# Performance work log

Hardware: AMD Instinct MI355X
Metric: run time of the kernel (lower is better)

Reference implementation:

```python
import jax, jax.numpy as jnp
import numpy as np

# ---- static config (mirrors GptOssDecoderLayer init) ----
H = 1024      # hidden_size
HD = 64       # head_size
NQ = 16       # num_query_heads
NKV = 4       # num_key_value_heads
G = NQ // NKV # num_key_value_groups
E = 8         # num_experts
TOPK = 2      # experts_per_token
FFN = 1024    # expert intermediate (== hidden in GPT-OSS)
B, Q = 4, 128 # batch sequences, new query tokens per sequence
P, PS = 8, 128
S = P * PS    # kv length per sequence
T = B * Q     # total query tokens
SW = 128      # sliding window (layer_idx % 2 == 0 -> active)
LIMIT = 7.0   # swiglu_limit
ALPHA = 1.702
EPS = 1e-5
NEG = -1e30
SCALE = HD ** -0.5


def rmsnorm(x, w):
    return x * w * jax.lax.rsqrt(jnp.mean(x * x, axis=-1, keepdims=True) + EPS)


def setup_inputs() -> dict:
    key = jax.random.key(0)
    ks = jax.random.split(key, 16)
    hidden = jax.random.normal(ks[0], (T, H), jnp.float32)
    kv_cache = jax.random.normal(ks[1], (B * P, 2, PS, NKV, HD), jnp.float32)
    kv_page_indices = jnp.arange(B * P, dtype=jnp.int32).reshape(B, P)
    # additive causal mask: query q sits at absolute position S - Q + q
    qpos = S - Q + jnp.arange(Q)
    kpos = jnp.arange(S)
    causal = qpos[:, None] >= kpos[None, :]
    attention_mask = jnp.broadcast_to(
        jnp.where(causal, 0.0, NEG).astype(jnp.float32), (B, Q, S))
    sinks = 0.1 * jax.random.normal(ks[2], (NQ,), jnp.float32)
    w_qkv = jax.random.normal(ks[3], (H, HD * (NQ + 2 * NKV)), jnp.float32) / np.sqrt(H)
    b_qkv = jnp.zeros((HD * (NQ + 2 * NKV),), jnp.float32)
    w_o = jax.random.normal(ks[4], (NQ * HD, H), jnp.float32) / np.sqrt(NQ * HD)
    b_o = jnp.zeros((H,), jnp.float32)
    ln1_w = jnp.ones((H,), jnp.float32)
    ln2_w = jnp.ones((H,), jnp.float32)
    w_router = jax.random.normal(ks[5], (H, E), jnp.float32) / np.sqrt(H)
    b_router = jnp.zeros((E,), jnp.float32)
    w_gate_up = jax.random.normal(ks[6], (E, H, 2 * FFN), jnp.float32) / np.sqrt(H)
    b_gate_up = jnp.zeros((E, 2 * FFN), jnp.float32)
    w_down = jax.random.normal(ks[7], (E, FFN, H), jnp.float32) / np.sqrt(FFN)
    b_down = jnp.zeros((E, H), jnp.float32)
    return dict(hidden=hidden, kv_cache=kv_cache, attention_mask=attention_mask,
                kv_page_indices=kv_page_indices, sinks=sinks, w_qkv=w_qkv,
                b_qkv=b_qkv, w_o=w_o, b_o=b_o, ln1_w=ln1_w, ln2_w=ln2_w,
                w_router=w_router, b_router=b_router, w_gate_up=w_gate_up,
                b_gate_up=b_gate_up, w_down=w_down, b_down=b_down)


def reference(hidden, kv_cache, attention_mask, kv_page_indices, sinks,
              w_qkv, b_qkv, w_o, b_o, ln1_w, ln2_w, w_router, b_router,
              w_gate_up, b_gate_up, w_down, b_down):
    # ---- attention block ----
    x = rmsnorm(hidden, ln1_w)
    qkv = x @ w_qkv + b_qkv                       # [T, HD*(NQ+2*NKV)]
    q = qkv[:, :NQ * HD].reshape(B, Q, NQ, HD)
    k_new = qkv[:, NQ * HD:(NQ + NKV) * HD].reshape(B, Q, NKV, HD)
    v_new = qkv[:, (NQ + NKV) * HD:].reshape(B, Q, NKV, HD)
    # gather paged KV cache -> [B, S, NKV, HD]; write new tokens into tail slots
    pages = kv_cache[kv_page_indices]             # [B, P, 2, PS, NKV, HD]
    K = pages[:, :, 0].reshape(B, S, NKV, HD).at[:, S - Q:].set(k_new)
    V = pages[:, :, 1].reshape(B, S, NKV, HD).at[:, S - Q:].set(v_new)
    Kr = jnp.repeat(K, G, axis=2)                 # GQA expand -> [B, S, NQ, HD]
    Vr = jnp.repeat(V, G, axis=2)
    scores = jnp.einsum('bqhd,bshd->bhqs', q * SCALE, Kr) + attention_mask[:, None]
    # sliding-window (module trims pages outside the window; equivalent mask)
    qpos = S - Q + jnp.arange(Q)
    kpos = jnp.arange(S)
    win_ok = (qpos[:, None] - kpos[None, :]) < SW
    scores = jnp.where(win_ok[None, None], scores, NEG)
    m = jnp.max(scores, axis=-1)
    m = jnp.where(jnp.isinf(m) & (m < 0), 0.0, m)
    p = jnp.exp(scores - m[..., None])            # [B, NQ, Q, S]
    # attention sink joins the softmax denominator (online-softmax correction)
    denom = jnp.sum(p, axis=-1) + jnp.exp(sinks[None, :, None] - m)
    attn = jnp.einsum('bhqs,bshd->bhqd', p, Vr) / denom[..., None]
    attn = attn.transpose(0, 2, 1, 3).reshape(T, NQ * HD)
    h = hidden + attn @ w_o + b_o
    # ---- MoE block ----
    x2 = rmsnorm(h, ln2_w)
    logits = x2 @ w_router + b_router             # [T, E]
    vals, idx = jax.lax.top_k(logits, TOPK)
    wts = jax.nn.softmax(vals, axis=-1)
    comb = jnp.sum(jax.nn.one_hot(idx, E, dtype=x2.dtype) * wts[..., None], axis=1)
    gu = jnp.einsum('th,ehf->etf', x2, w_gate_up) + b_gate_up[:, None, :]
    gate = jnp.minimum(gu[..., 0::2], LIMIT)
    up = jnp.clip(gu[..., 1::2], -LIMIT, LIMIT)
    glu = gate * jax.nn.sigmoid(gate * ALPHA)
    eo = jnp.einsum('etf,efh->eth', (up + 1.0) * glu, w_down) + b_down[:, None, :]
    moe = jnp.einsum('te,eth->th', comb, eo)
    return h + moe
```

## Files before the change

kernel.cpp:

```cpp
#include <hip/hip_runtime.h>

constexpr int H    = 1024;
constexpr int HD   = 64;
constexpr int NQ   = 16;
constexpr int NKV  = 4;
constexpr int E_   = 8;
constexpr int FFN  = 1024;
constexpr int B_   = 4;
constexpr int Q_   = 128;
constexpr int P_   = 8;
constexpr int PS   = 128;
constexpr int S_   = P_ * PS;
constexpr int T_   = B_ * Q_;
constexpr int QKV_N = HD * (NQ + 2 * NKV);
constexpr float EPS   = 1e-5f;
constexpr float ALPHA = 1.702f;
constexpr float LIMIT = 7.0f;
constexpr float SCALE = 0.125f;

constexpr int MAXROWS = 1536;
constexpr int MAXTILES = 24;

typedef __attribute__((ext_vector_type(4))) float f32x4;
typedef __attribute__((ext_vector_type(8))) short s16x8;

__device__ __forceinline__ unsigned short f2bf(float f) {
    unsigned u = __float_as_uint(f);
    u += 0x7FFFu + ((u >> 16) & 1u);
    return (unsigned short)(u >> 16);
}

__device__ __forceinline__ void lds_barrier() {
    asm volatile("s_waitcnt lgkmcnt(0)" ::: "memory");
    __builtin_amdgcn_s_barrier();
}

__global__ __launch_bounds__(256) void rmsnorm_kernel(const float* __restrict__ in,
                                                      const float* __restrict__ w,
                                                      unsigned short* __restrict__ outb,
                                                      int* __restrict__ cnt) {
    int t   = blockIdx.x;
    int tid = threadIdx.x;
    if (t == 0 && tid < E_) cnt[tid] = 0;
    float4 v = ((const float4*)(in + (size_t)t * H))[tid];
    float ss = v.x * v.x + v.y * v.y + v.z * v.z + v.w * v.w;
#pragma unroll
    for (int off = 32; off; off >>= 1) ss += __shfl_down(ss, off);
    __shared__ float partial[4];
    __shared__ float s_inv;
    if ((tid & 63) == 0) partial[tid >> 6] = ss;
    __syncthreads();
    if (tid == 0)
        s_inv = rsqrtf((partial[0] + partial[1] + partial[2] + partial[3]) * (1.0f / H) + EPS);
    __syncthreads();
    float inv = s_inv;
    float4 wv = ((const float4*)w)[tid];
    ushort4 ob;
    ob.x = f2bf(v.x * wv.x * inv); ob.y = f2bf(v.y * wv.y * inv);
    ob.z = f2bf(v.z * wv.z * inv); ob.w = f2bf(v.w * wv.w * inv);
    ((ushort4*)(outb + (size_t)t * H))[tid] = ob;
}

#define GPHASE(LDSR, LDSW, WRW, WRI, TI, NT, AFD0, AFD1, TA, AFS0, AFS1, STRIDE)      \
    {                                                                                  \
        s16x8 b00 = *(const s16x8*)&LDSR[kq][r16][0];                                  \
        s16x8 b01 = *(const s16x8*)&LDSR[kq][16 + r16][0];                             \
        s16x8 b10 = *(const s16x8*)&LDSR[4 + kq][r16][0];                              \
        s16x8 b11 = *(const s16x8*)&LDSR[4 + kq][16 + r16][0];                         \
        if (TA < NT) {                                                                 \
            AFD0 = *(const s16x8*)(ap + (TA) * 64);                                    \
            AFD1 = *(const s16x8*)(ap + (TA) * 64 + 32);                               \
        }                                                                              \
        if (TI < NT) {                                                                 \
            _Pragma("unroll")                                                          \
            for (int j = 0; j < 8; j++) WRI[j] = wsrc[(size_t)((TI) * 64 + j) * STRIDE]; \
        }                                                                              \
        acc0 = __builtin_amdgcn_mfma_f32_16x16x32_bf16(AFS0, b00, acc0, 0, 0, 0);      \
        acc1 = __builtin_amdgcn_mfma_f32_16x16x32_bf16(AFS0, b01, acc1, 0, 0, 0);      \
        acc0 = __builtin_amdgcn_mfma_f32_16x16x32_bf16(AFS1, b10, acc0, 0, 0, 0);      \
        acc1 = __builtin_amdgcn_mfma_f32_16x16x32_bf16(AFS1, b11, acc1, 0, 0, 0);      \
        if (TI - 3 < NT) {                                                             \
            s16x8 p;                                                                   \
            _Pragma("unroll")                                                          \
            for (int j = 0; j < 8; j++) p[j] = (short)f2bf(WRW[j]);                    \
            *(s16x8*)&LDSW[skb][sn][0] = p;                                            \
        }                                                                              \
        lds_barrier();                                                                 \
    }

#define GPROLOGUE(NT, STRIDE)                                                          \
    float wr0[8], wr1[8], wr2[8], wr3[8], wrP[8];                                      \
    s16x8 afA0, afA1, afB0, afB1;                                                      \
    f32x4 acc0 = {}, acc1 = {};                                                        \
    _Pragma("unroll")                                                                  \
    for (int j = 0; j < 8; j++) wrP[j] = wsrc[(size_t)j * STRIDE];                     \
    _Pragma("unroll")                                                                  \
    for (int j = 0; j < 8; j++) wr0[j] = wsrc[(size_t)(64 + j) * STRIDE];              \
    if (2 < NT) { _Pragma("unroll")                                                    \
        for (int j = 0; j < 8; j++) wr1[j] = wsrc[(size_t)(128 + j) * STRIDE]; }       \
    if (3 < NT) { _Pragma("unroll")                                                    \
        for (int j = 0; j < 8; j++) wr2[j] = wsrc[(size_t)(192 + j) * STRIDE]; }       \
    {                                                                                  \
        s16x8 p;                                                                       \
        _Pragma("unroll")                                                              \
        for (int j = 0; j < 8; j++) p[j] = (short)f2bf(wrP[j]);                        \
        *(s16x8*)&WtA[skb][sn][0] = p;                                                 \
    }                                                                                  \
    afA0 = *(const s16x8*)(ap);                                                        \
    afA1 = *(const s16x8*)(ap + 32);                                                   \
    lds_barrier();

#define GQUAD(T, NT, STRIDE)                                                           \
    GPHASE(WtA, WtB, wr0, wr3, (T) + 4, NT, afB0, afB1, (T) + 1, afA0, afA1, STRIDE)   \
    GPHASE(WtB, WtA, wr1, wr0, (T) + 5, NT, afA0, afA1, (T) + 2, afB0, afB1, STRIDE)   \
    GPHASE(WtA, WtB, wr2, wr1, (T) + 6, NT, afB0, afB1, (T) + 3, afA0, afA1, STRIDE)   \
    GPHASE(WtB, WtA, wr3, wr2, (T) + 7, NT, afA0, afA1, (T) + 4, afB0, afB1, STRIDE)

__global__ __launch_bounds__(256) void gemm_dense_t(const unsigned short* __restrict__ Abf,
                                                    const float* __restrict__ W,
                                                    const float* __restrict__ bias,
                                                    const float* __restrict__ resid,
                                                    float* __restrict__ C,
                                                    float* __restrict__ Cdup, int N) {
    int nb = blockIdx.x, mb = blockIdx.y * 64;
    int tid = threadIdx.x;
    int w = tid >> 6, lane = tid & 63;
    int r16 = lane & 15, kq = lane >> 4;
    int skb = tid >> 5, sn = tid & 31;

    __shared__ unsigned short WtA[8][32][8];
    __shared__ unsigned short WtB[8][32][8];

    size_t sN = (size_t)N;
    const float* wsrc = W + (size_t)(skb * 8) * sN + nb * 32 + sn;
    const unsigned short* ap = Abf + (size_t)(mb + w * 16 + r16) * 1024 + kq * 8;

    GPROLOGUE(16, sN)
#pragma unroll
    for (int i = 0; i < 4; i++) {
        GQUAD(4 * i, 16, sN)
    }

    int row0 = mb + w * 16 + kq * 4;
    f32x4 accs[2] = {acc0, acc1};
#pragma unroll
    for (int nf = 0; nf < 2; nf++) {
        int col = nb * 32 + nf * 16 + r16;
        float bcol = bias[col];
#pragma unroll
        for (int r = 0; r < 4; r++) {
            int row = row0 + r;
            float v = accs[nf][r] + bcol;
            if (resid) v += resid[(size_t)row * sN + col];
            C[(size_t)row * sN + col] = v;
            if (Cdup) Cdup[(size_t)row * sN + col] = v;
        }
    }
}

__global__ __launch_bounds__(256) void attn_group_kernel(const float* __restrict__ qkv,
                                                         const float* __restrict__ kv_cache,
                                                         const int* __restrict__ page_idx,
                                                         const float* __restrict__ sinks,
                                                         unsigned short* __restrict__ attn_bf) {
    int blk = blockIdx.x;
    int kvh = blk & 3;
    int q   = (blk >> 2) & 127;
    int b   = blk >> 9;
    int t   = b * Q_ + q;
    int tid = threadIdx.x;
    int s_lo = S_ - Q_ - 127 + q;

    __shared__ __align__(16) float Vs[128][64];
    __shared__ __align__(16) float qs4[4][64];
    __shared__ float pv[4][128];
    __shared__ float sD[4];

#pragma unroll
    for (int r = 0; r < 8; r++) {
        int l = r * 256 + tid;
        int key = l >> 4, c = l & 15;
        int s = s_lo + key;
        const float* vp;
        if (s < S_ - Q_) {
            int page = page_idx[b * P_ + (s >> 7)];
            vp = kv_cache + (size_t)page * 65536 + 32768 + (size_t)(s & 127) * (NKV * HD) + kvh * HD;
        } else {
            vp = qkv + (size_t)(b * Q_ + (s - (S_ - Q_))) * QKV_N + (NQ + NKV) * HD + kvh * HD;
        }
        ((float4*)Vs[key])[c] = *(const float4*)(vp + c * 4);
    }
    {
        int hh = tid >> 6, d2 = tid & 63;
        qs4[hh][d2] = qkv[(size_t)t * QKV_N + (kvh * 4 + hh) * HD + d2];
    }
    __syncthreads();

    {
        int key = tid & 127, hp = tid >> 7;
        int s = s_lo + key;
        const float* kp;
        if (s < S_ - Q_) {
            int page = page_idx[b * P_ + (s >> 7)];
            kp = kv_cache + (size_t)page * 65536 + (size_t)(s & 127) * (NKV * HD) + kvh * HD;
        } else {
            kp = qkv + (size_t)(b * Q_ + (s - (S_ - Q_))) * QKV_N + NQ * HD + kvh * HD;
        }
        const float4* kp4 = (const float4*)kp;
        const float4* q0p = (const float4*)qs4[hp * 2];
        const float4* q1p = (const float4*)qs4[hp * 2 + 1];
        float sc0 = 0.f, sc1 = 0.f;
#pragma unroll
        for (int d4 = 0; d4 < 16; d4++) {
            float4 kk = kp4[d4];
            float4 q0 = q0p[d4], q1 = q1p[d4];
            sc0 += q0.x * kk.x + q0.y * kk.y + q0.z * kk.z + q0.w * kk.w;
            sc1 += q1.x * kk.x + q1.y * kk.y + q1.z * kk.z + q1.w * kk.w;
        }
        pv[hp * 2][key]     = sc0 * SCALE;
        pv[hp * 2 + 1][key] = sc1 * SCALE;
    }
    __syncthreads();

    {
        int wv = tid >> 6, lane = tid & 63;
        float a0 = pv[wv][lane], a1 = pv[wv][lane + 64];
        float m = fmaxf(a0, a1);
#pragma unroll
        for (int off = 32; off; off >>= 1) m = fmaxf(m, __shfl_xor(m, off));
        float p0 = __expf(a0 - m), p1 = __expf(a1 - m);
        float l = p0 + p1;
#pragma unroll
        for (int off = 32; off; off >>= 1) l += __shfl_xor(l, off);
        pv[wv][lane] = p0;
        pv[wv][lane + 64] = p1;
        if (lane == 0) sD[wv] = l + __expf(sinks[kvh * 4 + wv] - m);
    }
    __syncthreads();

    {
        int hh = tid >> 6, d2 = tid & 63;
        float a0 = 0.f, a1 = 0.f, a2 = 0.f, a3 = 0.f;
#pragma unroll 4
        for (int i = 0; i < 128; i += 4) {
            a0 += pv[hh][i]     * Vs[i][d2];
            a1 += pv[hh][i + 1] * Vs[i + 1][d2];
            a2 += pv[hh][i + 2] * Vs[i + 2][d2];
            a3 += pv[hh][i + 3] * Vs[i + 3][d2];
        }
        float acc = ((a0 + a1) + (a2 + a3)) / sD[hh];
        attn_bf[(size_t)t * (NQ * HD) + (kvh * 4 + hh) * HD + d2] = f2bf(acc);
    }
}

__global__ __launch_bounds__(256) void rms_router_kernel(const float* __restrict__ hbuf,
                                                         const float* __restrict__ ln2w,
                                                         const float* __restrict__ w_router,
                                                         const float* __restrict__ b_router,
                                                         unsigned short* __restrict__ x2bf,
                                                         int* __restrict__ ridx,
                                                         float* __restrict__ rwt,
                                                         int* __restrict__ cnt) {
    int t = blockIdx.x;
    int tid = threadIdx.x;
    float4 v = ((const float4*)(hbuf + (size_t)t * H))[tid];
    float ss = v.x * v.x + v.y * v.y + v.z * v.z + v.w * v.w;
#pragma unroll
    for (int off = 32; off; off >>= 1) ss += __shfl_down(ss, off);
    __shared__ float partial[4];
    __shared__ float s_inv;
    if ((tid & 63) == 0) partial[tid >> 6] = ss;
    __syncthreads();
    if (tid == 0)
        s_inv = rsqrtf((partial[0] + partial[1] + partial[2] + partial[3]) * (1.0f / H) + EPS);
    __syncthreads();
    float inv = s_inv;
    float4 wv = ((const float4*)ln2w)[tid];
    float4 o;
    o.x = v.x * wv.x * inv; o.y = v.y * wv.y * inv;
    o.z = v.z * wv.z * inv; o.w = v.w * wv.w * inv;
    ushort4 ob;
    ob.x = f2bf(o.x); ob.y = f2bf(o.y); ob.z = f2bf(o.z); ob.w = f2bf(o.w);
    ((ushort4*)(x2bf + (size_t)t * H))[tid] = ob;

    const float4* wr = (const float4*)(w_router + (size_t)tid * 4 * E_);
    float p[E_];
    {
        float4 r0a = wr[0], r0b = wr[1];
        float4 r1a = wr[2], r1b = wr[3];
        float4 r2a = wr[4], r2b = wr[5];
        float4 r3a = wr[6], r3b = wr[7];
        p[0] = o.x * r0a.x + o.y * r1a.x + o.z * r2a.x + o.w * r3a.x;
        p[1] = o.x * r0a.y + o.y * r1a.y + o.z * r2a.y + o.w * r3a.y;
        p[2] = o.x * r0a.z + o.y * r1a.z + o.z * r2a.z + o.w * r3a.z;
        p[3] = o.x * r0a.w + o.y * r1a.w + o.z * r2a.w + o.w * r3a.w;
        p[4] = o.x * r0b.x + o.y * r1b.x + o.z * r2b.x + o.w * r3b.x;
        p[5] = o.x * r0b.y + o.y * r1b.y + o.z * r2b.y + o.w * r3b.y;
        p[6] = o.x * r0b.z + o.y * r1b.z + o.z * r2b.z + o.w * r3b.z;
        p[7] = o.x * r0b.w + o.y * r1b.w + o.z * r2b.w + o.w * r3b.w;
    }
    __shared__ float wsum[4][E_];
    int wv2 = tid >> 6, lane = tid & 63;
#pragma unroll
    for (int e = 0; e < E_; e++) {
        float r = p[e];
#pragma unroll
        for (int off = 32; off; off >>= 1) r += __shfl_xor(r, off);
        if (lane == 0) wsum[wv2][e] = r;
    }
    __syncthreads();
    __shared__ float logits[E_];
    if (tid < E_)
        logits[tid] = wsum[0][tid] + wsum[1][tid] + wsum[2][tid] + wsum[3][tid] + b_router[tid];
    __syncthreads();
    if (tid == 0) {
        int i0 = 0; float v0 = logits[0];
        for (int ee = 1; ee < E_; ee++)
            if (logits[ee] > v0) { v0 = logits[ee]; i0 = ee; }
        int i1 = -1; float v1 = -3.4e38f;
        for (int ee = 0; ee < E_; ee++)
            if (ee != i0 && logits[ee] > v1) { v1 = logits[ee]; i1 = ee; }
        float w0 = 1.0f / (1.0f + __expf(v1 - v0));
        ridx[t * 2] = i0; ridx[t * 2 + 1] = i1;
        rwt[t * 2] = w0;  rwt[t * 2 + 1] = 1.0f - w0;
        atomicAdd(&cnt[i0], 1);
        atomicAdd(&cnt[i1], 1);
    }
}

__global__ __launch_bounds__(256) void plumb_kernel(const int* __restrict__ cnt,
                                                    const int* __restrict__ ridx,
                                                    int* __restrict__ poff,
                                                    int* __restrict__ list,
                                                    int* __restrict__ tmap) {
    __shared__ int lpos[E_], lpoff[E_];
    int tid = threadIdx.x;
    if (tid == 0) {
        int run = 0, it = 0;
        for (int e = 0; e < E_; e++) {
            lpoff[e] = run; poff[e] = run;
            int pc = (cnt[e] + 63) & ~63;
            for (int tl = 0; tl < (pc >> 6); tl++) tmap[1 + it++] = (e << 5) | tl;
            run += pc;
        }
        tmap[0] = it;
    }
    if (tid < E_) lpos[tid] = 0;
    __syncthreads();
    for (int i = tid; i < 2 * T_; i += 256) {
        int e = ridx[i];
        int pp = atomicAdd(&lpos[e], 1);
        list[lpoff[e] + pp] = i;
    }
}

__global__ __launch_bounds__(256) void moe_gateup_t(const unsigned short* __restrict__ x2bf,
                                                    const int* __restrict__ list,
                                                    const int* __restrict__ cnt,
                                                    const int* __restrict__ poff,
                                                    const int* __restrict__ tmap,
                                                    const float* __restrict__ wgu,
                                                    const float* __restrict__ bgu,
                                                    unsigned short* __restrict__ act_bf) {
    if ((int)blockIdx.y >= tmap[0]) return;
    int v0m = tmap[1 + blockIdx.y];
    int e = v0m >> 5, tl = v0m & 31;
    int n = cnt[e];
    int base = poff[e];
    int nb = blockIdx.x;
    int tid = threadIdx.x;
    int w = tid >> 6, lane = tid & 63;
    int r16 = lane & 15, kq = lane >> 4;
    int skb = tid >> 5, sn = tid & 31;

    __shared__ unsigned short WtA[8][32][8];
    __shared__ unsigned short WtB[8][32][8];

    const float* wsrc = wgu + (size_t)e * (1024 * 2048) + (size_t)(skb * 8) * 2048 + nb * 32 + sn;
    int rr0 = tl * 64 + w * 16 + r16;
    int t2a = (rr0 < n) ? list[base + rr0] : list[base];
    const unsigned short* ap = x2bf + (size_t)(t2a >> 1) * 1024 + kq * 8;

    GPROLOGUE(16, 2048)
#pragma unroll
    for (int i = 0; i < 4; i++) {
        GQUAD(4 * i, 16, 2048)
    }

    int parity = r16 & 1;
    f32x4 accs[2] = {acc0, acc1};
#pragma unroll
    for (int nf = 0; nf < 2; nf++) {
        int gucol = nb * 32 + nf * 16 + r16;
        float bb = bgu[(size_t)e * 2048 + gucol];
#pragma unroll
        for (int r = 0; r < 4; r++) {
            float v = accs[nf][r] + bb;
            float o = __shfl_xor(v, 1);
            if (!parity) {
                float g = fminf(v, LIMIT);
                float u = fminf(fmaxf(o, -LIMIT), LIMIT);
                float glu = g / (1.0f + __expf(-ALPHA * g));
                int rr = tl * 64 + w * 16 + kq * 4 + r;
                if (rr < n)
                    act_bf[(size_t)(base + rr) * FFN + (gucol >> 1)] = f2bf((u + 1.0f) * glu);
            }
        }
    }
}

__global__ __launch_bounds__(256) void moe_down_t(const unsigned short* __restrict__ act_bf,
                                                  const int* __restrict__ list,
                                                  const int* __restrict__ cnt,
                                                  const int* __restrict__ poff,
                                                  const int* __restrict__ tmap,
                                                  const float* __restrict__ rwt,
                                                  const float* __restrict__ wdn,
                                                  const float* __restrict__ b_down,
                                                  float* __restrict__ out) {
    if ((int)blockIdx.y >= tmap[0]) return;
    int v0m = tmap[1 + blockIdx.y];
    int e = v0m >> 5, tl = v0m & 31;
    int n = cnt[e];
    int base = poff[e];
    int nb = blockIdx.x;
    int z  = blockIdx.z;
    int tid = threadIdx.x;
    int w = tid >> 6, lane = tid & 63;
    int r16 = lane & 15, kq = lane >> 4;
    int skb = tid >> 5, sn = tid & 31;

    __shared__ unsigned short WtA[8][32][8];
    __shared__ unsigned short WtB[8][32][8];

    const float* wsrc = wdn + (size_t)e * (1024 * 1024) + (size_t)(z * 512 + skb * 8) * 1024 + nb * 32 + sn;
    const unsigned short* ap = act_bf + (size_t)(base + tl * 64 + w * 16 + r16) * 1024 + z * 512 + kq * 8;

    GPROLOGUE(8, 1024)
#pragma unroll
    for (int i = 0; i < 2; i++) {
        GQUAD(4 * i, 8, 1024)
    }

    f32x4 accs[2] = {acc0, acc1};
#pragma unroll
    for (int r = 0; r < 4; r++) {
        int rr = tl * 64 + w * 16 + kq * 4 + r;
        if (rr < n) {
            int t2 = list[base + rr];
            float sc = rwt[t2];
            float* op = out + (size_t)(t2 >> 1) * H;
#pragma unroll
            for (int nf = 0; nf < 2; nf++) {
                int col = nb * 32 + nf * 16 + r16;
                float v = accs[nf][r] + (z == 0 ? b_down[(size_t)e * 1024 + col] : 0.0f);
                atomicAdd(op + col, sc * v);
            }
        }
    }
}

extern "C" void kernel_launch(void* const* d_in, const int* in_sizes, int n_in,
                              void* d_out, int out_size, void* d_ws, size_t ws_size,
                              hipStream_t stream) {
    const float* hidden          = (const float*)d_in[0];
    const float* kv_cache        = (const float*)d_in[1];
    const int*   kv_page_indices = (const int*)d_in[3];
    const float* sinks           = (const float*)d_in[4];
    const float* w_qkv           = (const float*)d_in[5];
    const float* b_qkv           = (const float*)d_in[6];
    const float* w_o             = (const float*)d_in[7];
    const float* b_o             = (const float*)d_in[8];
    const float* ln1_w           = (const float*)d_in[9];
    const float* ln2_w           = (const float*)d_in[10];
    const float* w_router        = (const float*)d_in[11];
    const float* b_router        = (const float*)d_in[12];
    const float* w_gate_up       = (const float*)d_in[13];
    const float* b_gate_up       = (const float*)d_in[14];
    const float* w_down          = (const float*)d_in[15];
    const float* b_down          = (const float*)d_in[16];
    float* out = (float*)d_out;

    char* base = (char*)d_ws;
    float* qkv   = (float*)base;                       base += (size_t)T_ * QKV_N * 4;
    float* hbuf  = (float*)base;                       base += (size_t)T_ * H * 4;
    unsigned short* x_bf    = (unsigned short*)base;   base += (size_t)T_ * H * 2;
    unsigned short* x2_bf   = (unsigned short*)base;   base += (size_t)T_ * H * 2;
    unsigned short* attn_bf = (unsigned short*)base;   base += (size_t)T_ * NQ * HD * 2;
    unsigned short* act_bf  = (unsigned short*)base;   base += (size_t)(MAXROWS + 128) * FFN * 2;
    float* rwt  = (float*)base;                        base += 2 * T_ * 4;
    int*   ridx = (int*)base;                          base += 2 * T_ * 4;
    int*   cnt  = (int*)base;                          base += E_ * 4;
    int*   poff = (int*)base;                          base += E_ * 4;
    int*   list = (int*)base;                          base += MAXROWS * 4;
    int*   tmap = (int*)base;                          base += (1 + MAXTILES + 7) * 4;

    rmsnorm_kernel<<<T_, 256, 0, stream>>>(hidden, ln1_w, x_bf, cnt);
    gemm_dense_t<<<dim3(QKV_N / 32, T_ / 64), 256, 0, stream>>>(
        x_bf, w_qkv, b_qkv, nullptr, qkv, nullptr, QKV_N);
    attn_group_kernel<<<B_ * Q_ * NKV, 256, 0, stream>>>(qkv, kv_cache, kv_page_indices, sinks, attn_bf);
    gemm_dense_t<<<dim3(H / 32, T_ / 64), 256, 0, stream>>>(
        attn_bf, w_o, b_o, hidden, hbuf, out, H);
    rms_router_kernel<<<T_, 256, 0, stream>>>(hbuf, ln2_w, w_router, b_router,
                                              x2_bf, ridx, rwt, cnt);
    plumb_kernel<<<1, 256, 0, stream>>>(cnt, ridx, poff, list, tmap);
    moe_gateup_t<<<dim3(FFN * 2 / 32, MAXTILES), 256, 0, stream>>>(
        x2_bf, list, cnt, poff, tmap, w_gate_up, b_gate_up, act_bf);
    moe_down_t<<<dim3(H / 32, MAXTILES, 2), 256, 0, stream>>>(
        act_bf, list, cnt, poff, tmap, rwt, w_down, b_down, out);
}
```

Measured before the change: 278.0 us.

## Stage GEMM tiles via direct global-to-LDS loads with swizzled double buffering

Result: slower. 285.0 us (+2.5%).

```diff
diff --git a/kernel.cpp b/kernel.cpp
--- a/kernel.cpp
+++ b/kernel.cpp
@@ -30,10 +30,49 @@
     return (unsigned short)(u >> 16);
 }
 
-__device__ __forceinline__ void lds_barrier() {
-    asm volatile("s_waitcnt lgkmcnt(0)" ::: "memory");
+typedef __attribute__((address_space(3))) void lds_void;
+typedef __attribute__((address_space(1))) void glb_void;
+__device__ __forceinline__ void stage16(const void* g, void* l) {
+    __builtin_amdgcn_global_load_lds((const glb_void*)g, (lds_void*)l, 16, 0, 0);
+}
+
+__device__ __forceinline__ void phase_barrier() {
+    asm volatile("s_waitcnt vmcnt(0) lgkmcnt(0)" ::: "memory");
     __builtin_amdgcn_s_barrier();
 }
+
+#define COMPUTE(ABUF, WBUF)                                                                   \
+    {                                                                                         \
+        const char* Ab = (const char*)(ABUF);                                                 \
+        s16x8 a0 = *(const s16x8*)(Ab + arow_off + aseg0 * 16);                               \
+        s16x8 a1 = *(const s16x8*)(Ab + arow_off + aseg1 * 16);                               \
+        const float* w0 = (const float*)(WBUF) + wbase0;                                      \
+        const float* w1 = (const float*)(WBUF) + wbase1;                                      \
+        float t0[8], t1[8], t2[8], t3[8];                                                     \
+        _Pragma("unroll")                                                                     \
+        for (int j = 0; j < 8; j++) {                                                         \
+            t0[j] = w0[j * 32];        t1[j] = w1[j * 32];                                    \
+            t2[j] = w0[1024 + j * 32]; t3[j] = w1[1024 + j * 32];                             \
+        }                                                                                     \
+        s16x8 b00, b01, b10, b11;                                                             \
+        _Pragma("unroll")                                                                     \
+        for (int j = 0; j < 8; j++) {                                                         \
+            b00[j] = (short)f2bf(t0[j]); b01[j] = (short)f2bf(t1[j]);                         \
+            b10[j] = (short)f2bf(t2[j]); b11[j] = (short)f2bf(t3[j]);                         \
+        }                                                                                     \
+        acc0 = __builtin_amdgcn_mfma_f32_16x16x32_bf16(a0, b00, acc0, 0, 0, 0);               \
+        acc1 = __builtin_amdgcn_mfma_f32_16x16x32_bf16(a0, b01, acc1, 0, 0, 0);               \
+        acc0 = __builtin_amdgcn_mfma_f32_16x16x32_bf16(a1, b10, acc0, 0, 0, 0);               \
+        acc1 = __builtin_amdgcn_mfma_f32_16x16x32_bf16(a1, b11, acc1, 0, 0, 0);               \
+    }
+
+#define FRAG_SETUP                                                                            \
+    int arow_off = (w * 16 + r16) * 128;                                                      \
+    int aseg0 = kq ^ (r16 & 7);                                                               \
+    int aseg1 = (kq | 4) ^ (r16 & 7);                                                         \
+    int wsw = (kq & 1) << 4;                                                                  \
+    int wbase0 = kq * 256 + (r16 ^ wsw);                                                      \
+    int wbase1 = kq * 256 + ((16 + r16) ^ wsw);
 
 __global__ __launch_bounds__(256) void rmsnorm_kernel(const float* __restrict__ in,
                                                       const float* __restrict__ w,
@@ -60,61 +99,6 @@
     ob.z = f2bf(v.z * wv.z * inv); ob.w = f2bf(v.w * wv.w * inv);
     ((ushort4*)(outb + (size_t)t * H))[tid] = ob;
 }
-
-#define GPHASE(LDSR, LDSW, WRW, WRI, TI, NT, AFD0, AFD1, TA, AFS0, AFS1, STRIDE)      \
-    {                                                                                  \
-        s16x8 b00 = *(const s16x8*)&LDSR[kq][r16][0];                                  \
-        s16x8 b01 = *(const s16x8*)&LDSR[kq][16 + r16][0];                             \
-        s16x8 b10 = *(const s16x8*)&LDSR[4 + kq][r16][0];                              \
-        s16x8 b11 = *(const s16x8*)&LDSR[4 + kq][16 + r16][0];                         \
-        if (TA < NT) {                                                                 \
-            AFD0 = *(const s16x8*)(ap + (TA) * 64);                                    \
-            AFD1 = *(const s16x8*)(ap + (TA) * 64 + 32);                               \
-        }                                                                              \
-        if (TI < NT) {                                                                 \
-            _Pragma("unroll")                                                          \
-            for (int j = 0; j < 8; j++) WRI[j] = wsrc[(size_t)((TI) * 64 + j) * STRIDE]; \
-        }                                                                              \
-        acc0 = __builtin_amdgcn_mfma_f32_16x16x32_bf16(AFS0, b00, acc0, 0, 0, 0);      \
-        acc1 = __builtin_amdgcn_mfma_f32_16x16x32_bf16(AFS0, b01, acc1, 0, 0, 0);      \
-        acc0 = __builtin_amdgcn_mfma_f32_16x16x32_bf16(AFS1, b10, acc0, 0, 0, 0);      \
-        acc1 = __builtin_amdgcn_mfma_f32_16x16x32_bf16(AFS1, b11, acc1, 0, 0, 0);      \
-        if (TI - 3 < NT) {                                                             \
-            s16x8 p;                                                                   \
-            _Pragma("unroll")                                                          \
-            for (int j = 0; j < 8; j++) p[j] = (short)f2bf(WRW[j]);                    \
-            *(s16x8*)&LDSW[skb][sn][0] = p;                                            \
-        }                                                                              \
-        lds_barrier();                                                                 \
-    }
-
-#define GPROLOGUE(NT, STRIDE)                                                          \
-    float wr0[8], wr1[8], wr2[8], wr3[8], wrP[8];                                      \
-    s16x8 afA0, afA1, afB0, afB1;                                                      \
-    f32x4 acc0 = {}, acc1 = {};                                                        \
-    _Pragma("unroll")                                                                  \
-    for (int j = 0; j < 8; j++) wrP[j] = wsrc[(size_t)j * STRIDE];                     \
-    _Pragma("unroll")                                                                  \
-    for (int j = 0; j < 8; j++) wr0[j] = wsrc[(size_t)(64 + j) * STRIDE];              \
-    if (2 < NT) { _Pragma("unroll")                                                    \
-        for (int j = 0; j < 8; j++) wr1[j] = wsrc[(size_t)(128 + j) * STRIDE]; }       \
-    if (3 < NT) { _Pragma("unroll")                                                    \
-        for (int j = 0; j < 8; j++) wr2[j] = wsrc[(size_t)(192 + j) * STRIDE]; }       \
-    {                                                                                  \
-        s16x8 p;                                                                       \
-        _Pragma("unroll")                                                              \
-        for (int j = 0; j < 8; j++) p[j] = (short)f2bf(wrP[j]);                        \
-        *(s16x8*)&WtA[skb][sn][0] = p;                                                 \
-    }                                                                                  \
-    afA0 = *(const s16x8*)(ap);                                                        \
-    afA1 = *(const s16x8*)(ap + 32);                                                   \
-    lds_barrier();
-
-#define GQUAD(T, NT, STRIDE)                                                           \
-    GPHASE(WtA, WtB, wr0, wr3, (T) + 4, NT, afB0, afB1, (T) + 1, afA0, afA1, STRIDE)   \
-    GPHASE(WtB, WtA, wr1, wr0, (T) + 5, NT, afA0, afA1, (T) + 2, afB0, afB1, STRIDE)   \
-    GPHASE(WtA, WtB, wr2, wr1, (T) + 6, NT, afB0, afB1, (T) + 3, afA0, afA1, STRIDE)   \
-    GPHASE(WtB, WtA, wr3, wr2, (T) + 7, NT, afA0, afA1, (T) + 4, afB0, afB1, STRIDE)
 
 __global__ __launch_bounds__(256) void gemm_dense_t(const unsigned short* __restrict__ Abf,
                                                     const float* __restrict__ W,
@@ -126,22 +110,47 @@
     int tid = threadIdx.x;
     int w = tid >> 6, lane = tid & 63;
     int r16 = lane & 15, kq = lane >> 4;
-    int skb = tid >> 5, sn = tid & 31;
-
-    __shared__ unsigned short WtA[8][32][8];
-    __shared__ unsigned short WtB[8][32][8];
+
+    __shared__ __align__(16) char AfA[8192], AfB[8192], WfA[8192], WfB[8192];
 
     size_t sN = (size_t)N;
-    const float* wsrc = W + (size_t)(skb * 8) * sN + nb * 32 + sn;
-    const unsigned short* ap = Abf + (size_t)(mb + w * 16 + r16) * 1024 + kq * 8;
-
-    GPROLOGUE(16, sN)
-#pragma unroll
-    for (int i = 0; i < 4; i++) {
-        GQUAD(4 * i, 16, sN)
-    }
-
-    int row0 = mb + w * 16 + kq * 4;
+    int row0  = tid >> 3;
+    int ss    = (tid & 7) ^ (row0 & 7);
+    int wcol  = nb * 32 + (((tid & 7) * 4) ^ (((tid >> 6) & 1) << 4));
+    int wvofs = (tid >> 6) * 1024;
+
+    const unsigned short* pA0 = Abf + (size_t)(mb + row0) * 1024 + ss * 8;
+    const unsigned short* pA1 = pA0 + 32 * 1024;
+
+    FRAG_SETUP
+    f32x4 acc0 = {}, acc1 = {};
+
+    auto stageA = [&](char* dst, int T) {
+        stage16(pA0 + T * 64, dst + wvofs);
+        stage16(pA1 + T * 64, dst + wvofs + 4096);
+    };
+    auto stageW = [&](char* dst, int T) {
+        stage16(W + (size_t)(T * 64 + row0) * sN + wcol, dst + wvofs);
+        stage16(W + (size_t)(T * 64 + row0 + 32) * sN + wcol, dst + wvofs + 4096);
+    };
+
+    stageA(AfA, 0); stageW(WfA, 0);
+    phase_barrier();
+#pragma unroll
+    for (int s = 0; s < 8; ++s) {
+        stageA(AfB, 2 * s + 1); stageW(WfB, 2 * s + 1);
+        __builtin_amdgcn_sched_barrier(0);
+        COMPUTE(AfA, WfA)
+        phase_barrier();
+        if (2 * s + 2 < 16) {
+            stageA(AfA, 2 * s + 2); stageW(WfA, 2 * s + 2);
+            __builtin_amdgcn_sched_barrier(0);
+        }
+        COMPUTE(AfB, WfB)
+        phase_barrier();
+    }
+
+    int row0e = mb + w * 16 + kq * 4;
     f32x4 accs[2] = {acc0, acc1};
 #pragma unroll
     for (int nf = 0; nf < 2; nf++) {
@@ -149,7 +158,7 @@
         float bcol = bias[col];
 #pragma unroll
         for (int r = 0; r < 4; r++) {
-            int row = row0 + r;
+            int row = row0e + r;
             float v = accs[nf][r] + bcol;
             if (resid) v += resid[(size_t)row * sN + col];
             C[(size_t)row * sN + col] = v;
@@ -371,20 +380,48 @@
     int tid = threadIdx.x;
     int w = tid >> 6, lane = tid & 63;
     int r16 = lane & 15, kq = lane >> 4;
-    int skb = tid >> 5, sn = tid & 31;
-
-    __shared__ unsigned short WtA[8][32][8];
-    __shared__ unsigned short WtB[8][32][8];
-
-    const float* wsrc = wgu + (size_t)e * (1024 * 2048) + (size_t)(skb * 8) * 2048 + nb * 32 + sn;
-    int rr0 = tl * 64 + w * 16 + r16;
-    int t2a = (rr0 < n) ? list[base + rr0] : list[base];
-    const unsigned short* ap = x2bf + (size_t)(t2a >> 1) * 1024 + kq * 8;
-
-    GPROLOGUE(16, 2048)
-#pragma unroll
-    for (int i = 0; i < 4; i++) {
-        GQUAD(4 * i, 16, 2048)
+
+    __shared__ __align__(16) char AfA[8192], AfB[8192], WfA[8192], WfB[8192];
+
+    int row0  = tid >> 3;
+    int ss    = (tid & 7) ^ (row0 & 7);
+    int wcol  = nb * 32 + (((tid & 7) * 4) ^ (((tid >> 6) & 1) << 4));
+    int wvofs = (tid >> 6) * 1024;
+
+    const float* Wg = wgu + (size_t)e * (1024 * 2048);
+    int rr0 = tl * 64 + row0;
+    int rr1 = rr0 + 32;
+    int tok0 = (rr0 < n) ? list[base + rr0] : list[base];
+    int tok1 = (rr1 < n) ? list[base + rr1] : list[base];
+    const unsigned short* pA0 = x2bf + (size_t)(tok0 >> 1) * 1024 + ss * 8;
+    const unsigned short* pA1 = x2bf + (size_t)(tok1 >> 1) * 1024 + ss * 8;
+
+    FRAG_SETUP
+    f32x4 acc0 = {}, acc1 = {};
+
+    auto stageA = [&](char* dst, int T) {
+        stage16(pA0 + T * 64, dst + wvofs);
+        stage16(pA1 + T * 64, dst + wvofs + 4096);
+    };
+    auto stageW = [&](char* dst, int T) {
+        stage16(Wg + (size_t)(T * 64 + row0) * 2048 + wcol, dst + wvofs);
+        stage16(Wg + (size_t)(T * 64 + row0 + 32) * 2048 + wcol, dst + wvofs + 4096);
+    };
+
+    stageA(AfA, 0); stageW(WfA, 0);
+    phase_barrier();
+#pragma unroll
+    for (int s = 0; s < 8; ++s) {
+        stageA(AfB, 2 * s + 1); stageW(WfB, 2 * s + 1);
+        __builtin_amdgcn_sched_barrier(0);
+        COMPUTE(AfA, WfA)
+        phase_barrier();
+        if (2 * s + 2 < 16) {
+            stageA(AfA, 2 * s + 2); stageW(WfA, 2 * s + 2);
+            __builtin_amdgcn_sched_barrier(0);
+        }
+        COMPUTE(AfB, WfB)
+        phase_barrier();
     }
 
     int parity = r16 & 1;
@@ -428,18 +465,44 @@
     int tid = threadIdx.x;
     int w = tid >> 6, lane = tid & 63;
     int r16 = lane & 15, kq = lane >> 4;
-    int skb = tid >> 5, sn = tid & 31;
-
-    __shared__ unsigned short WtA[8][32][8];
-    __shared__ unsigned short WtB[8][32][8];
-
-    const float* wsrc = wdn + (size_t)e * (1024 * 1024) + (size_t)(z * 512 + skb * 8) * 1024 + nb * 32 + sn;
-    const unsigned short* ap = act_bf + (size_t)(base + tl * 64 + w * 16 + r16) * 1024 + z * 512 + kq * 8;
-
-    GPROLOGUE(8, 1024)
-#pragma unroll
-    for (int i = 0; i < 2; i++) {
-        GQUAD(4 * i, 8, 1024)
+
+    __shared__ __align__(16) char AfA[8192], AfB[8192], WfA[8192], WfB[8192];
+
+    int row0  = tid >> 3;
+    int ss    = (tid & 7) ^ (row0 & 7);
+    int wcol  = nb * 32 + (((tid & 7) * 4) ^ (((tid >> 6) & 1) << 4));
+    int wvofs = (tid >> 6) * 1024;
+
+    const float* Wg = wdn + (size_t)e * (1024 * 1024) + (size_t)(z * 512) * 1024;
+    const unsigned short* pA0 = act_bf + (size_t)(base + tl * 64 + row0) * 1024 + z * 512 + ss * 8;
+    const unsigned short* pA1 = pA0 + 32 * 1024;
+
+    FRAG_SETUP
+    f32x4 acc0 = {}, acc1 = {};
+
+    auto stageA = [&](char* dst, int T) {
+        stage16(pA0 + T * 64, dst + wvofs);
+        stage16(pA1 + T * 64, dst + wvofs + 4096);
+    };
+    auto stageW = [&](char* dst, int T) {
+        stage16(Wg + (size_t)(T * 64 + row0) * 1024 + wcol, dst + wvofs);
+        stage16(Wg + (size_t)(T * 64 + row0 + 32) * 1024 + wcol, dst + wvofs + 4096);
+    };
+
+    stageA(AfA, 0); stageW(WfA, 0);
+    phase_barrier();
+#pragma unroll
+    for (int s = 0; s < 4; ++s) {
+        stageA(AfB, 2 * s + 1); stageW(WfB, 2 * s + 1);
+        __builtin_amdgcn_sched_barrier(0);
+        COMPUTE(AfA, WfA)
+        phase_barrier();
+        if (2 * s + 2 < 8) {
+            stageA(AfA, 2 * s + 2); stageW(WfA, 2 * s + 2);
+            __builtin_amdgcn_sched_barrier(0);
+        }
+        COMPUTE(AfB, WfB)
+        phase_barrier();
     }
 
     f32x4 accs[2] = {acc0, acc1};
```
